# Kernel tuning notes

Measured on AMD Instinct MI355X. Metric: run time of the kernel, lower is better.

Reference implementation:

```python
import jax, jax.numpy as jnp
import numpy as np

B, V, P, N = 8, 4096, 2048, 32
IN_DIM, H, D, L = 256, 8, 32, 2
MLP, RES = 128, 100
HD = H * D
EPS = 1e-5


def setup_inputs() -> dict:
    key = jax.random.key(0)
    ks = jax.random.split(key, 12)
    s = 0.02
    inp = {
        'encoded': jax.random.normal(ks[0], (B, V, IN_DIM), jnp.float32),
        'true_u': jax.random.uniform(ks[1], (B, V), jnp.float32),
        'pred_points': jax.random.randint(ks[2], (P,), 0, V),
        'neighbor_index': jax.random.randint(ks[3], (P, N), 0, V),
        'Wds': s * jax.random.normal(ks[4], (IN_DIM, HD), jnp.float32),
        'bds': jnp.zeros((HD,), jnp.float32),
    }

    def mlp_params(k, lead, in_dim, out_dim):
        kk = jax.random.split(k, 3)
        return (s * jax.random.normal(kk[0], lead + (in_dim, MLP), jnp.float32), jnp.zeros(lead + (MLP,), jnp.float32),
                s * jax.random.normal(kk[1], lead + (MLP, MLP), jnp.float32), jnp.zeros(lead + (MLP,), jnp.float32),
                s * jax.random.normal(kk[2], lead + (MLP, out_dim), jnp.float32), jnp.zeros(lead + (out_dim,), jnp.float32))

    inp['kW1'], inp['kb1'], inp['kW2'], inp['kb2'], inp['kW3'], inp['kb3'] = mlp_params(ks[5], (L, H), IN_DIM + 1, D)
    inp['vW1'], inp['vb1'], inp['vW2'], inp['vb2'], inp['vW3'], inp['vb3'] = mlp_params(ks[6], (L, H), IN_DIM + 1, D)
    inp['dW1'], inp['db1'], inp['dW2'], inp['db2'], inp['dW3'], inp['db3'] = mlp_params(ks[7], (), HD, RES)
    inp['ln1_g'] = jnp.ones((L, HD), jnp.float32); inp['ln1_b'] = jnp.zeros((L, HD), jnp.float32)
    inp['ln2_g'] = jnp.ones((L, HD), jnp.float32); inp['ln2_b'] = jnp.zeros((L, HD), jnp.float32)
    inp['fW1'] = s * jax.random.normal(ks[8], (L, HD, HD), jnp.float32); inp['fb1'] = jnp.zeros((L, HD), jnp.float32)
    inp['fW2'] = s * jax.random.normal(ks[9], (L, HD, HD), jnp.float32); inp['fb2'] = jnp.zeros((L, HD), jnp.float32)
    return inp


def _ln(x, g, b):
    m = x.mean(-1, keepdims=True)
    v = ((x - m) ** 2).mean(-1, keepdims=True)
    return (x - m) * jax.lax.rsqrt(v + EPS) * g + b


def _per_head_mlp(x, W1, b1, W2, b2, W3, b3):
    # x: [B,V,I]; W1: [H,I,M] -> out [B,H,V,D]; all H per-head MLPs batched in one einsum
    h = jax.nn.relu(jnp.einsum('bvi,him->bhvm', x, W1) + b1[None, :, None, :])
    h = jax.nn.relu(jnp.einsum('bhvm,hmn->bhvn', h, W2) + b2[None, :, None, :])
    return jnp.einsum('bhvm,hmd->bhvd', h, W3) + b3[None, :, None, :]


def reference(encoded, true_u, pred_points, neighbor_index, Wds, bds, kW1, kb1, kW2, kb2, kW3, kb3, vW1, vb1, vW2, vb2, vW3, vb3, dW1, db1, dW2, db2, dW3, db3, ln1_g, ln1_b, ln2_g, ln2_b, fW1, fb1, fW2, fb2):
    merged = jnp.concatenate([encoded, true_u[..., None]], axis=-1)  # [B,V,IN+1]
    att_value = encoded[:, pred_points, :] @ Wds + bds               # [B,P,HD]
    scale = D ** -0.5
    for l in range(L):
        keys = _per_head_mlp(merged, kW1[l], kb1[l], kW2[l], kb2[l], kW3[l], kb3[l])    # [B,H,V,D]
        values = _per_head_mlp(merged, vW1[l], vb1[l], vW2[l], vb2[l], vW3[l], vb3[l])  # [B,H,V,D]
        nk = keys[:, :, neighbor_index, :]    # gather -> [B,H,P,N,D]
        nv = values[:, :, neighbor_index, :]
        q = att_value.reshape(att_value.shape[0], -1, H, D)  # [B,P,H,D]
        scores = scale * jnp.einsum('bphd,bhpnd->bphn', q, nk)
        w = jax.nn.softmax(scores, axis=-1)
        att = jnp.einsum('bphn,bhpnd->bphd', w, nv).reshape(att_value.shape)
        att_value = _ln(att_value + att, ln1_g[l], ln1_b[l])
        ff = jax.nn.relu(att_value @ fW1[l] + fb1[l]) @ fW2[l] + fb2[l]
        att_value = _ln(att_value + ff, ln2_g[l], ln2_b[l])
    h = jax.nn.relu(att_value @ dW1 + db1)
    h = jax.nn.relu(h @ dW2 + db2)
    logits = h @ dW3 + db3  # [B,P,RES]
    target = jnp.clip(jnp.floor(true_u[..., None] * RES).astype(jnp.int32), 0, RES - 1)  # [B,V,1]
    logprob = jnp.log(jnp.float32(RES)) + jax.nn.log_softmax(logits, axis=2)
    picked = jnp.take_along_axis(logprob, target[:, pred_points, :], axis=2)  # [B,P,1]
    return -picked.sum((1, 2))  # [B]
```

## Files before the change

### kernel.cpp

```cpp
#include <hip/hip_runtime.h>
#include <math.h>

#define B_    8
#define V_    4096
#define P_    2048
#define N_    32
#define INDIM 256
#define H_    8
#define D_    32
#define L_    2
#define MLP_  128
#define RES_  100
#define HD_   256
#define EPS_  1e-5f
#define SCALE_ 0.17677669529663687f
#define LOG_RES_ 4.605170185988091f

__global__ __launch_bounds__(256) void k_init_att(
    const float* __restrict__ encoded, const int* __restrict__ pp,
    const float* __restrict__ Wds, const float* __restrict__ bds,
    float* __restrict__ att)
{
    __shared__ float xs[32][INDIM];
    const int t = threadIdx.x;
    const int g0 = blockIdx.x * 32;
    for (int idx = t; idx < 32 * INDIM; idx += 256) {
        int r = idx >> 8, i = idx & 255;
        int g = g0 + r;
        int b = g >> 11, pl = g & 2047;
        xs[r][i] = encoded[((size_t)b * V_ + pp[pl]) * INDIM + i];
    }
    __syncthreads();
    const int jg = t & 63, rg = t >> 6;
    const int j = jg * 4;
    float acc[8][4];
    #pragma unroll
    for (int r = 0; r < 8; ++r)
        #pragma unroll
        for (int c = 0; c < 4; ++c) acc[r][c] = 0.f;
    for (int i = 0; i < INDIM; ++i) {
        const float4 w = *(const float4*)&Wds[(size_t)i * HD_ + j];
        #pragma unroll
        for (int r = 0; r < 8; ++r) {
            float x = xs[rg * 8 + r][i];
            acc[r][0] += x * w.x; acc[r][1] += x * w.y;
            acc[r][2] += x * w.z; acc[r][3] += x * w.w;
        }
    }
    const float4 bb = *(const float4*)&bds[j];
    #pragma unroll
    for (int r = 0; r < 8; ++r) {
        float4 o;
        o.x = acc[r][0] + bb.x; o.y = acc[r][1] + bb.y;
        o.z = acc[r][2] + bb.z; o.w = acc[r][3] + bb.w;
        *(float4*)&att[((size_t)(g0 + rg * 8 + r)) * HD_ + j] = o;
    }
}

__global__ __launch_bounds__(256) void k_kv_mlp(
    const float* __restrict__ encoded, const float* __restrict__ true_u,
    const float* __restrict__ kW1, const float* __restrict__ kb1,
    const float* __restrict__ kW2, const float* __restrict__ kb2,
    const float* __restrict__ kW3, const float* __restrict__ kb3,
    const float* __restrict__ vW1, const float* __restrict__ vb1,
    const float* __restrict__ vW2, const float* __restrict__ vb2,
    const float* __restrict__ vW3, const float* __restrict__ vb3,
    float* __restrict__ keys, float* __restrict__ values)
{
    __shared__ float smem[32 * (INDIM + 1) + 32 * (MLP_ + 1)];
    float (*xs)[INDIM + 1] = (float (*)[INDIM + 1])smem;
    float (*h1)[MLP_ + 1]  = (float (*)[MLP_ + 1])(smem + 32 * (INDIM + 1));
    float (*h2)[MLP_ + 1]  = (float (*)[MLP_ + 1])smem;

    const int t  = threadIdx.x;
    const int g0 = blockIdx.x * 32;
    const int b  = g0 >> 12;
    const int v0 = g0 & (V_ - 1);
    const int hh = blockIdx.y;
    const int kv = blockIdx.z;
    const float* W1 = (kv ? vW1 : kW1) + (size_t)hh * (INDIM + 1) * MLP_;
    const float* b1 = (kv ? vb1 : kb1) + hh * MLP_;
    const float* W2 = (kv ? vW2 : kW2) + (size_t)hh * MLP_ * MLP_;
    const float* b2 = (kv ? vb2 : kb2) + hh * MLP_;
    const float* W3 = (kv ? vW3 : kW3) + (size_t)hh * MLP_ * D_;
    const float* b3 = (kv ? vb3 : kb3) + hh * D_;
    float* outp = kv ? values : keys;

    const float* xb = encoded + ((size_t)b * V_ + v0) * INDIM;
    for (int idx = t; idx < 32 * INDIM; idx += 256) {
        int r = idx >> 8, i = idx & 255;
        xs[r][i] = xb[(size_t)r * INDIM + i];
    }
    if (t < 32) xs[t][INDIM] = true_u[(size_t)b * V_ + v0 + t];
    __syncthreads();

    const int cg = t & 31;
    const int vg = t >> 5;

    {
        const int m = cg * 4;
        float acc[4][4];
        #pragma unroll
        for (int r = 0; r < 4; ++r)
            #pragma unroll
            for (int c = 0; c < 4; ++c) acc[r][c] = 0.f;
        for (int i = 0; i < INDIM + 1; ++i) {
            const float4 w = *(const float4*)&W1[(size_t)i * MLP_ + m];
            #pragma unroll
            for (int r = 0; r < 4; ++r) {
                float x = xs[vg * 4 + r][i];
                acc[r][0] += x * w.x; acc[r][1] += x * w.y;
                acc[r][2] += x * w.z; acc[r][3] += x * w.w;
            }
        }
        const float4 bb = *(const float4*)&b1[m];
        #pragma unroll
        for (int r = 0; r < 4; ++r) {
            h1[vg * 4 + r][m + 0] = fmaxf(acc[r][0] + bb.x, 0.f);
            h1[vg * 4 + r][m + 1] = fmaxf(acc[r][1] + bb.y, 0.f);
            h1[vg * 4 + r][m + 2] = fmaxf(acc[r][2] + bb.z, 0.f);
            h1[vg * 4 + r][m + 3] = fmaxf(acc[r][3] + bb.w, 0.f);
        }
    }
    __syncthreads();

    {
        const int m = cg * 4;
        float acc[4][4];
        #pragma unroll
        for (int r = 0; r < 4; ++r)
            #pragma unroll
            for (int c = 0; c < 4; ++c) acc[r][c] = 0.f;
        for (int i = 0; i < MLP_; ++i) {
            const float4 w = *(const float4*)&W2[(size_t)i * MLP_ + m];
            #pragma unroll
            for (int r = 0; r < 4; ++r) {
                float x = h1[vg * 4 + r][i];
                acc[r][0] += x * w.x; acc[r][1] += x * w.y;
                acc[r][2] += x * w.z; acc[r][3] += x * w.w;
            }
        }
        const float4 bb = *(const float4*)&b2[m];
        #pragma unroll
        for (int r = 0; r < 4; ++r) {
            h2[vg * 4 + r][m + 0] = fmaxf(acc[r][0] + bb.x, 0.f);
            h2[vg * 4 + r][m + 1] = fmaxf(acc[r][1] + bb.y, 0.f);
            h2[vg * 4 + r][m + 2] = fmaxf(acc[r][2] + bb.z, 0.f);
            h2[vg * 4 + r][m + 3] = fmaxf(acc[r][3] + bb.w, 0.f);
        }
    }
    __syncthreads();

    {
        const int dg = t & 7;
        const int vq = t >> 3;
        const int d = dg * 4;
        float acc[4] = {0.f, 0.f, 0.f, 0.f};
        for (int i = 0; i < MLP_; ++i) {
            const float4 w = *(const float4*)&W3[(size_t)i * D_ + d];
            float x = h2[vq][i];
            acc[0] += x * w.x; acc[1] += x * w.y;
            acc[2] += x * w.z; acc[3] += x * w.w;
        }
        float4 o;
        o.x = acc[0] + b3[d + 0]; o.y = acc[1] + b3[d + 1];
        o.z = acc[2] + b3[d + 2]; o.w = acc[3] + b3[d + 3];
        *(float4*)&outp[((size_t)b * V_ + v0 + vq) * HD_ + hh * D_ + d] = o;
    }
}

__global__ __launch_bounds__(256) void k_attn_ln(
    const float* __restrict__ keys, const float* __restrict__ values,
    const int* __restrict__ nbr,
    const float* __restrict__ g, const float* __restrict__ bet,
    float* __restrict__ att)
{
    __shared__ float qs[HD_];
    __shared__ float ws[H_][N_];
    __shared__ int   idx[N_];
    __shared__ float red[4];
    const int t = threadIdx.x;
    const int bp = blockIdx.x;
    const int b = bp >> 11;
    const int p = bp & (P_ - 1);
    if (t < N_) idx[t] = nbr[p * N_ + t];
    qs[t] = att[(size_t)bp * HD_ + t];
    __syncthreads();

    const int hh = t >> 5;
    {
        const int n = t & 31;
        const float4* kp = (const float4*)(keys + ((size_t)b * V_ + idx[n]) * HD_ + hh * D_);
        float s = 0.f;
        #pragma unroll
        for (int j = 0; j < 8; ++j) {
            const float4 kk = kp[j];
            s += qs[hh * D_ + j * 4 + 0] * kk.x + qs[hh * D_ + j * 4 + 1] * kk.y +
                 qs[hh * D_ + j * 4 + 2] * kk.z + qs[hh * D_ + j * 4 + 3] * kk.w;
        }
        s *= SCALE_;
        float m = s;
        #pragma unroll
        for (int off = 16; off; off >>= 1) m = fmaxf(m, __shfl_xor(m, off, 32));
        float e = expf(s - m);
        float sum = e;
        #pragma unroll
        for (int off = 16; off; off >>= 1) sum += __shfl_xor(sum, off, 32);
        ws[hh][n] = e / sum;
    }
    __syncthreads();

    float a = 0.f;
    {
        const int d = t & 31;
        const float* vb = values + (size_t)b * V_ * HD_ + hh * D_ + d;
        #pragma unroll
        for (int n2 = 0; n2 < N_; ++n2)
            a += ws[hh][n2] * vb[(size_t)idx[n2] * HD_];
    }

    float x = qs[t] + a;
    float s1 = x;
    #pragma unroll
    for (int off = 32; off; off >>= 1) s1 += __shfl_xor(s1, off, 64);
    if ((t & 63) == 0) red[t >> 6] = s1;
    __syncthreads();
    float mean = (red[0] + red[1] + red[2] + red[3]) * (1.f / HD_);
    __syncthreads();
    float dx = x - mean;
    float v2 = dx * dx;
    #pragma unroll
    for (int off = 32; off; off >>= 1) v2 += __shfl_xor(v2, off, 64);
    if ((t & 63) == 0) red[t >> 6] = v2;
    __syncthreads();
    float var = (red[0] + red[1] + red[2] + red[3]) * (1.f / HD_);
    att[(size_t)bp * HD_ + t] = dx * rsqrtf(var + EPS_) * g[t] + bet[t];
}

#define FP_ (HD_ + 4)
__global__ __launch_bounds__(256) void k_ff_ln(
    const float* __restrict__ W1, const float* __restrict__ b1,
    const float* __restrict__ W2, const float* __restrict__ b2,
    const float* __restrict__ g, const float* __restrict__ bet,
    float* __restrict__ att)
{
    __shared__ float xs[32][FP_];
    __shared__ float hs[32][FP_];
    const int t = threadIdx.x;
    const int g0 = blockIdx.x * 32;
    for (int idx = t; idx < 32 * HD_; idx += 256) {
        int r = idx >> 8, i = idx & 255;
        xs[r][i] = att[((size_t)(g0 + r)) * HD_ + i];
    }
    __syncthreads();
    const int jg = t & 63, rg = t >> 6;
    const int j = jg * 4;

    float acc[8][4];
    #pragma unroll
    for (int r = 0; r < 8; ++r)
        #pragma unroll
        for (int c = 0; c < 4; ++c) acc[r][c] = 0.f;
    for (int i = 0; i < HD_; ++i) {
        const float4 w = *(const float4*)&W1[(size_t)i * HD_ + j];
        #pragma unroll
        for (int r = 0; r < 8; ++r) {
            float x = xs[rg * 8 + r][i];
            acc[r][0] += x * w.x; acc[r][1] += x * w.y;
            acc[r][2] += x * w.z; acc[r][3] += x * w.w;
        }
    }
    {
        const float4 bb = *(const float4*)&b1[j];
        #pragma unroll
        for (int r = 0; r < 8; ++r) {
            float4 o;
            o.x = fmaxf(acc[r][0] + bb.x, 0.f); o.y = fmaxf(acc[r][1] + bb.y, 0.f);
            o.z = fmaxf(acc[r][2] + bb.z, 0.f); o.w = fmaxf(acc[r][3] + bb.w, 0.f);
            *(float4*)&hs[rg * 8 + r][j] = o;
        }
    }
    __syncthreads();

    #pragma unroll
    for (int r = 0; r < 8; ++r)
        #pragma unroll
        for (int c = 0; c < 4; ++c) acc[r][c] = 0.f;
    for (int i = 0; i < HD_; ++i) {
        const float4 w = *(const float4*)&W2[(size_t)i * HD_ + j];
        #pragma unroll
        for (int r = 0; r < 8; ++r) {
            float x = hs[rg * 8 + r][i];
            acc[r][0] += x * w.x; acc[r][1] += x * w.y;
            acc[r][2] += x * w.z; acc[r][3] += x * w.w;
        }
    }
    float y[8][4];
    {
        const float4 bb = *(const float4*)&b2[j];
        #pragma unroll
        for (int r = 0; r < 8; ++r) {
            y[r][0] = acc[r][0] + bb.x + xs[rg * 8 + r][j + 0];
            y[r][1] = acc[r][1] + bb.y + xs[rg * 8 + r][j + 1];
            y[r][2] = acc[r][2] + bb.z + xs[rg * 8 + r][j + 2];
            y[r][3] = acc[r][3] + bb.w + xs[rg * 8 + r][j + 3];
        }
    }
    __syncthreads();
    #pragma unroll
    for (int r = 0; r < 8; ++r) {
        float4 o; o.x = y[r][0]; o.y = y[r][1]; o.z = y[r][2]; o.w = y[r][3];
        *(float4*)&xs[rg * 8 + r][j] = o;
    }
    __syncthreads();

    const int rr = t >> 3, k = t & 7;
    float s = 0.f;
    for (int i = 0; i < 32; ++i) s += xs[rr][k + 8 * i];
    #pragma unroll
    for (int off = 4; off; off >>= 1) s += __shfl_xor(s, off, 8);
    float mean = s * (1.f / HD_);
    float vs = 0.f;
    for (int i = 0; i < 32; ++i) { float d = xs[rr][k + 8 * i] - mean; vs += d * d; }
    #pragma unroll
    for (int off = 4; off; off >>= 1) vs += __shfl_xor(vs, off, 8);
    float rstd = rsqrtf(vs * (1.f / HD_) + EPS_);
    for (int i = 0; i < 32; ++i) {
        int jj = k + 8 * i;
        att[((size_t)(g0 + rr)) * HD_ + jj] =
            (xs[rr][jj] - mean) * rstd * g[jj] + bet[jj];
    }
}

__global__ __launch_bounds__(256) void k_dec_loss(
    const float* __restrict__ att, const float* __restrict__ true_u,
    const int* __restrict__ pp,
    const float* __restrict__ dW1, const float* __restrict__ db1,
    const float* __restrict__ dW2, const float* __restrict__ db2,
    const float* __restrict__ dW3, const float* __restrict__ db3,
    float* __restrict__ partial)
{
    __shared__ float xs[32][HD_];
    __shared__ float h1s[32][MLP_];
    __shared__ float h2s[32][MLP_];
    __shared__ float ls[32][104];
    __shared__ float rowloss[32];
    const int t = threadIdx.x;
    const int g0 = blockIdx.x * 32;
    for (int idx = t; idx < 32 * HD_; idx += 256) {
        int r = idx >> 8, i = idx & 255;
        xs[r][i] = att[((size_t)(g0 + r)) * HD_ + i];
    }
    __syncthreads();
    const int jg = t & 31, rg = t >> 5;
    const int j = jg * 4;

    {
        float acc[4][4];
        #pragma unroll
        for (int r = 0; r < 4; ++r)
            #pragma unroll
            for (int c = 0; c < 4; ++c) acc[r][c] = 0.f;
        for (int i = 0; i < HD_; ++i) {
            const float4 w = *(const float4*)&dW1[(size_t)i * MLP_ + j];
            #pragma unroll
            for (int r = 0; r < 4; ++r) {
                float x = xs[rg * 4 + r][i];
                acc[r][0] += x * w.x; acc[r][1] += x * w.y;
                acc[r][2] += x * w.z; acc[r][3] += x * w.w;
            }
        }
        const float4 bb = *(const float4*)&db1[j];
        #pragma unroll
        for (int r = 0; r < 4; ++r) {
            float4 o;
            o.x = fmaxf(acc[r][0] + bb.x, 0.f); o.y = fmaxf(acc[r][1] + bb.y, 0.f);
            o.z = fmaxf(acc[r][2] + bb.z, 0.f); o.w = fmaxf(acc[r][3] + bb.w, 0.f);
            *(float4*)&h1s[rg * 4 + r][j] = o;
        }
    }
    __syncthreads();
    {
        float acc[4][4];
        #pragma unroll
        for (int r = 0; r < 4; ++r)
            #pragma unroll
            for (int c = 0; c < 4; ++c) acc[r][c] = 0.f;
        for (int i = 0; i < MLP_; ++i) {
            const float4 w = *(const float4*)&dW2[(size_t)i * MLP_ + j];
            #pragma unroll
            for (int r = 0; r < 4; ++r) {
                float x = h1s[rg * 4 + r][i];
                acc[r][0] += x * w.x; acc[r][1] += x * w.y;
                acc[r][2] += x * w.z; acc[r][3] += x * w.w;
            }
        }
        const float4 bb = *(const float4*)&db2[j];
        #pragma unroll
        for (int r = 0; r < 4; ++r) {
            float4 o;
            o.x = fmaxf(acc[r][0] + bb.x, 0.f); o.y = fmaxf(acc[r][1] + bb.y, 0.f);
            o.z = fmaxf(acc[r][2] + bb.z, 0.f); o.w = fmaxf(acc[r][3] + bb.w, 0.f);
            *(float4*)&h2s[rg * 4 + r][j] = o;
        }
    }
    __syncthreads();
    {
        const bool act = (jg < 25);
        float acc[4][4];
        #pragma unroll
        for (int r = 0; r < 4; ++r)
            #pragma unroll
            for (int c = 0; c < 4; ++c) acc[r][c] = 0.f;
        for (int i = 0; i < MLP_; ++i) {
            float4 w = make_float4(0.f, 0.f, 0.f, 0.f);
            if (act) w = *(const float4*)&dW3[(size_t)i * RES_ + j];
            #pragma unroll
            for (int r = 0; r < 4; ++r) {
                float x = h2s[rg * 4 + r][i];
                acc[r][0] += x * w.x; acc[r][1] += x * w.y;
                acc[r][2] += x * w.z; acc[r][3] += x * w.w;
            }
        }
        if (act) {
            const float4 bb = *(const float4*)&db3[j];
            #pragma unroll
            for (int r = 0; r < 4; ++r) {
                ls[rg * 4 + r][j + 0] = acc[r][0] + bb.x;
                ls[rg * 4 + r][j + 1] = acc[r][1] + bb.y;
                ls[rg * 4 + r][j + 2] = acc[r][2] + bb.z;
                ls[rg * 4 + r][j + 3] = acc[r][3] + bb.w;
            }
        }
    }
    __syncthreads();

    const int rr = t >> 3, k = t & 7;
    float mx = -1e30f;
    for (int q = k; q < RES_; q += 8) mx = fmaxf(mx, ls[rr][q]);
    #pragma unroll
    for (int off = 4; off; off >>= 1) mx = fmaxf(mx, __shfl_xor(mx, off, 8));
    float se = 0.f;
    for (int q = k; q < RES_; q += 8) se += expf(ls[rr][q] - mx);
    #pragma unroll
    for (int off = 4; off; off >>= 1) se += __shfl_xor(se, off, 8);
    if (k == 0) {
        int gg = g0 + rr;
        int b = gg >> 11, pl = gg & (P_ - 1);
        float tu = true_u[(size_t)b * V_ + pp[pl]];
        int tgt = (int)floorf(tu * (float)RES_);
        tgt = tgt < 0 ? 0 : (tgt > RES_ - 1 ? RES_ - 1 : tgt);
        rowloss[rr] = LOG_RES_ + ls[rr][tgt] - mx - logf(se);
    }
    __syncthreads();
    if (t == 0) {
        float s = 0.f;
        for (int r2 = 0; r2 < 32; ++r2) s += rowloss[r2];
        partial[blockIdx.x] = -s;
    }
}

__global__ __launch_bounds__(64) void k_reduce_loss(
    const float* __restrict__ partial, float* __restrict__ loss)
{
    const int b = blockIdx.x, t = threadIdx.x;
    float s = partial[b * 64 + t];
    #pragma unroll
    for (int off = 32; off; off >>= 1) s += __shfl_xor(s, off, 64);
    if (t == 0) loss[b] = s;
}

extern "C" void kernel_launch(void* const* d_in, const int* in_sizes, int n_in,
                              void* d_out, int out_size, void* d_ws, size_t ws_size,
                              hipStream_t stream)
{
    (void)in_sizes; (void)n_in; (void)out_size; (void)ws_size;
    const float* encoded = (const float*)d_in[0];
    const float* true_u  = (const float*)d_in[1];
    const int*   pp      = (const int*)d_in[2];
    const int*   nbr     = (const int*)d_in[3];
    const float* Wds     = (const float*)d_in[4];
    const float* bds     = (const float*)d_in[5];
    const float* kW1 = (const float*)d_in[6];
    const float* kb1 = (const float*)d_in[7];
    const float* kW2 = (const float*)d_in[8];
    const float* kb2 = (const float*)d_in[9];
    const float* kW3 = (const float*)d_in[10];
    const float* kb3 = (const float*)d_in[11];
    const float* vW1 = (const float*)d_in[12];
    const float* vb1 = (const float*)d_in[13];
    const float* vW2 = (const float*)d_in[14];
    const float* vb2 = (const float*)d_in[15];
    const float* vW3 = (const float*)d_in[16];
    const float* vb3 = (const float*)d_in[17];
    const float* dW1 = (const float*)d_in[18];
    const float* db1 = (const float*)d_in[19];
    const float* dW2 = (const float*)d_in[20];
    const float* db2 = (const float*)d_in[21];
    const float* dW3 = (const float*)d_in[22];
    const float* db3 = (const float*)d_in[23];
    const float* ln1g = (const float*)d_in[24];
    const float* ln1b = (const float*)d_in[25];
    const float* ln2g = (const float*)d_in[26];
    const float* ln2b = (const float*)d_in[27];
    const float* fW1 = (const float*)d_in[28];
    const float* fb1 = (const float*)d_in[29];
    const float* fW2 = (const float*)d_in[30];
    const float* fb2 = (const float*)d_in[31];

    float* att  = (float*)d_ws;
    float* keys = att + (size_t)B_ * P_ * HD_;
    float* vals = keys + (size_t)B_ * V_ * HD_;
    float* part = vals + (size_t)B_ * V_ * HD_;

    k_init_att<<<dim3((B_ * P_) / 32), 256, 0, stream>>>(encoded, pp, Wds, bds, att);

    for (int l = 0; l < L_; ++l) {
        k_kv_mlp<<<dim3((B_ * V_) / 32, H_, 2), 256, 0, stream>>>(
            encoded, true_u,
            kW1 + (size_t)l * H_ * (INDIM + 1) * MLP_, kb1 + l * H_ * MLP_,
            kW2 + (size_t)l * H_ * MLP_ * MLP_,        kb2 + l * H_ * MLP_,
            kW3 + (size_t)l * H_ * MLP_ * D_,          kb3 + l * H_ * D_,
            vW1 + (size_t)l * H_ * (INDIM + 1) * MLP_, vb1 + l * H_ * MLP_,
            vW2 + (size_t)l * H_ * MLP_ * MLP_,        vb2 + l * H_ * MLP_,
            vW3 + (size_t)l * H_ * MLP_ * D_,          vb3 + l * H_ * D_,
            keys, vals);
        k_attn_ln<<<dim3(B_ * P_), 256, 0, stream>>>(
            keys, vals, nbr, ln1g + l * HD_, ln1b + l * HD_, att);
        k_ff_ln<<<dim3((B_ * P_) / 32), 256, 0, stream>>>(
            fW1 + (size_t)l * HD_ * HD_, fb1 + l * HD_,
            fW2 + (size_t)l * HD_ * HD_, fb2 + l * HD_,
            ln2g + l * HD_, ln2b + l * HD_, att);
    }

    k_dec_loss<<<dim3((B_ * P_) / 32), 256, 0, stream>>>(
        att, true_u, pp, dW1, db1, dW2, db2, dW3, db3, part);
    k_reduce_loss<<<dim3(B_), 64, 0, stream>>>(part, (float*)d_out);
}
```

Baseline: 2.796 ms.

## Restructure per-head KV MLP with float4 LDS reads, weight prefetch, halved shared memory

Rewrites the k_kv_mlp kernel so the 256-wide input is staged in two 128-column halves, with the second half held in registers. This shrinks shared memory and raises occupancy via launch_bounds(256,4). Inner loops now read four activations at once as float4 from a padded (132) LDS layout and software-prefetch the next four weight rows. The aim is fewer LDS instructions and hidden global weight-load latency. The trade-off is extra register pressure and an extra barrier for the second input half.

Result: faster. 2.597 ms (-7.1%).

```diff
diff --git a/kernel.cpp b/kernel.cpp
--- a/kernel.cpp
+++ b/kernel.cpp
@@ -16,6 +16,8 @@
 #define SCALE_ 0.17677669529663687f
 #define LOG_RES_ 4.605170185988091f
 
+#define LDP_  132
+
 __global__ __launch_bounds__(256) void k_init_att(
     const float* __restrict__ encoded, const int* __restrict__ pp,
     const float* __restrict__ Wds, const float* __restrict__ bds,
@@ -57,7 +59,38 @@
     }
 }
 
-__global__ __launch_bounds__(256) void k_kv_mlp(
+#define MLP_STEP4(XS, ROWBASE, ACC, I, WA, WB, WC, WD)                       \
+    { _Pragma("unroll")                                                      \
+      for (int r_ = 0; r_ < 4; ++r_) {                                       \
+        const float4 xv = *(const float4*)&XS[(ROWBASE) + r_][(I)];          \
+        ACC[r_][0] += xv.x*WA.x; ACC[r_][1] += xv.x*WA.y;                    \
+        ACC[r_][2] += xv.x*WA.z; ACC[r_][3] += xv.x*WA.w;                    \
+        ACC[r_][0] += xv.y*WB.x; ACC[r_][1] += xv.y*WB.y;                    \
+        ACC[r_][2] += xv.y*WB.z; ACC[r_][3] += xv.y*WB.w;                    \
+        ACC[r_][0] += xv.z*WC.x; ACC[r_][1] += xv.z*WC.y;                    \
+        ACC[r_][2] += xv.z*WC.z; ACC[r_][3] += xv.z*WC.w;                    \
+        ACC[r_][0] += xv.w*WD.x; ACC[r_][1] += xv.w*WD.y;                    \
+        ACC[r_][2] += xv.w*WD.z; ACC[r_][3] += xv.w*WD.w;                    \
+      } }
+
+#define PIPE128(WPTR, LDW, XS, ROWBASE, ACC)                                 \
+    { const float* wp_ = (WPTR);                                             \
+      float4 wa = *(const float4*)&wp_[0*(LDW)];                             \
+      float4 wb = *(const float4*)&wp_[1*(LDW)];                             \
+      float4 wc = *(const float4*)&wp_[2*(LDW)];                             \
+      float4 wd = *(const float4*)&wp_[3*(LDW)];                             \
+      for (int i_ = 0; i_ < 124; i_ += 4) {                                  \
+        float4 na = *(const float4*)&wp_[(size_t)(i_+4)*(LDW)];              \
+        float4 nb = *(const float4*)&wp_[(size_t)(i_+5)*(LDW)];              \
+        float4 nc = *(const float4*)&wp_[(size_t)(i_+6)*(LDW)];              \
+        float4 nd = *(const float4*)&wp_[(size_t)(i_+7)*(LDW)];              \
+        MLP_STEP4(XS, ROWBASE, ACC, i_, wa, wb, wc, wd);                     \
+        wa = na; wb = nb; wc = nc; wd = nd;                                  \
+      }                                                                      \
+      MLP_STEP4(XS, ROWBASE, ACC, 124, wa, wb, wc, wd);                      \
+    }
+
+__global__ __launch_bounds__(256, 4) void k_kv_mlp(
     const float* __restrict__ encoded, const float* __restrict__ true_u,
     const float* __restrict__ kW1, const float* __restrict__ kb1,
     const float* __restrict__ kW2, const float* __restrict__ kb2,
@@ -67,10 +100,12 @@
     const float* __restrict__ vW3, const float* __restrict__ vb3,
     float* __restrict__ keys, float* __restrict__ values)
 {
-    __shared__ float smem[32 * (INDIM + 1) + 32 * (MLP_ + 1)];
-    float (*xs)[INDIM + 1] = (float (*)[INDIM + 1])smem;
-    float (*h1)[MLP_ + 1]  = (float (*)[MLP_ + 1])(smem + 32 * (INDIM + 1));
-    float (*h2)[MLP_ + 1]  = (float (*)[MLP_ + 1])smem;
+    __shared__ float xcs[32 * LDP_];
+    __shared__ float h1s[32 * LDP_];
+    __shared__ float us[32];
+    float (*xc)[LDP_] = (float (*)[LDP_])xcs;
+    float (*h1)[LDP_] = (float (*)[LDP_])h1s;
+    float (*h2)[LDP_] = (float (*)[LDP_])xcs;
 
     const int t  = threadIdx.x;
     const int g0 = blockIdx.x * 32;
@@ -87,84 +122,110 @@
     float* outp = kv ? values : keys;
 
     const float* xb = encoded + ((size_t)b * V_ + v0) * INDIM;
-    for (int idx = t; idx < 32 * INDIM; idx += 256) {
-        int r = idx >> 8, i = idx & 255;
-        xs[r][i] = xb[(size_t)r * INDIM + i];
-    }
-    if (t < 32) xs[t][INDIM] = true_u[(size_t)b * V_ + v0 + t];
-    __syncthreads();
-
-    const int cg = t & 31;
-    const int vg = t >> 5;
-
-    {
-        const int m = cg * 4;
-        float acc[4][4];
-        #pragma unroll
-        for (int r = 0; r < 4; ++r)
-            #pragma unroll
-            for (int c = 0; c < 4; ++c) acc[r][c] = 0.f;
-        for (int i = 0; i < INDIM + 1; ++i) {
-            const float4 w = *(const float4*)&W1[(size_t)i * MLP_ + m];
-            #pragma unroll
-            for (int r = 0; r < 4; ++r) {
-                float x = xs[vg * 4 + r][i];
-                acc[r][0] += x * w.x; acc[r][1] += x * w.y;
-                acc[r][2] += x * w.z; acc[r][3] += x * w.w;
-            }
-        }
+    float4 c1r[4];
+    #pragma unroll
+    for (int k = 0; k < 4; ++k) {
+        int idx = t + (k << 8);
+        int row = idx >> 5, c4 = (idx & 31) << 2;
+        *(float4*)&xc[row][c4] = *(const float4*)&xb[(size_t)row * INDIM + c4];
+        c1r[k] = *(const float4*)&xb[(size_t)row * INDIM + 128 + c4];
+    }
+    if (t < 32) us[t] = true_u[(size_t)b * V_ + v0 + t];
+    __syncthreads();
+
+    const int cg = t & 31, vg = t >> 5;
+    const int m  = cg << 2;
+    const int r0 = vg << 2;
+
+    float acc[4][4];
+    #pragma unroll
+    for (int r = 0; r < 4; ++r)
+        #pragma unroll
+        for (int c = 0; c < 4; ++c) acc[r][c] = 0.f;
+
+    PIPE128(W1 + m, MLP_, xc, r0, acc);
+    __syncthreads();
+    #pragma unroll
+    for (int k = 0; k < 4; ++k) {
+        int idx = t + (k << 8);
+        int row = idx >> 5, c4 = (idx & 31) << 2;
+        *(float4*)&xc[row][c4] = c1r[k];
+    }
+    __syncthreads();
+    PIPE128(W1 + (size_t)128 * MLP_ + m, MLP_, xc, r0, acc);
+    {
+        const float4 wu = *(const float4*)&W1[(size_t)256 * MLP_ + m];
+        #pragma unroll
+        for (int r = 0; r < 4; ++r) {
+            float uu = us[r0 + r];
+            acc[r][0] += uu * wu.x; acc[r][1] += uu * wu.y;
+            acc[r][2] += uu * wu.z; acc[r][3] += uu * wu.w;
+        }
+    }
+    {
         const float4 bb = *(const float4*)&b1[m];
         #pragma unroll
         for (int r = 0; r < 4; ++r) {
-            h1[vg * 4 + r][m + 0] = fmaxf(acc[r][0] + bb.x, 0.f);
-            h1[vg * 4 + r][m + 1] = fmaxf(acc[r][1] + bb.y, 0.f);
-            h1[vg * 4 + r][m + 2] = fmaxf(acc[r][2] + bb.z, 0.f);
-            h1[vg * 4 + r][m + 3] = fmaxf(acc[r][3] + bb.w, 0.f);
-        }
-    }
-    __syncthreads();
-
-    {
-        const int m = cg * 4;
-        float acc[4][4];
-        #pragma unroll
-        for (int r = 0; r < 4; ++r)
-            #pragma unroll
-            for (int c = 0; c < 4; ++c) acc[r][c] = 0.f;
-        for (int i = 0; i < MLP_; ++i) {
-            const float4 w = *(const float4*)&W2[(size_t)i * MLP_ + m];
-            #pragma unroll
-            for (int r = 0; r < 4; ++r) {
-                float x = h1[vg * 4 + r][i];
-                acc[r][0] += x * w.x; acc[r][1] += x * w.y;
-                acc[r][2] += x * w.z; acc[r][3] += x * w.w;
-            }
-        }
+            float4 o;
+            o.x = fmaxf(acc[r][0] + bb.x, 0.f);
+            o.y = fmaxf(acc[r][1] + bb.y, 0.f);
+            o.z = fmaxf(acc[r][2] + bb.z, 0.f);
+            o.w = fmaxf(acc[r][3] + bb.w, 0.f);
+            *(float4*)&h1[r0 + r][m] = o;
+        }
+    }
+    __syncthreads();
+
+    #pragma unroll
+    for (int r = 0; r < 4; ++r)
+        #pragma unroll
+        for (int c = 0; c < 4; ++c) acc[r][c] = 0.f;
+    PIPE128(W2 + m, MLP_, h1, r0, acc);
+    {
         const float4 bb = *(const float4*)&b2[m];
         #pragma unroll
         for (int r = 0; r < 4; ++r) {
-            h2[vg * 4 + r][m + 0] = fmaxf(acc[r][0] + bb.x, 0.f);
-            h2[vg * 4 + r][m + 1] = fmaxf(acc[r][1] + bb.y, 0.f);
-            h2[vg * 4 + r][m + 2] = fmaxf(acc[r][2] + bb.z, 0.f);
-            h2[vg * 4 + r][m + 3] = fmaxf(acc[r][3] + bb.w, 0.f);
-        }
-    }
-    __syncthreads();
-
-    {
-        const int dg = t & 7;
-        const int vq = t >> 3;
-        const int d = dg * 4;
-        float acc[4] = {0.f, 0.f, 0.f, 0.f};
-        for (int i = 0; i < MLP_; ++i) {
-            const float4 w = *(const float4*)&W3[(size_t)i * D_ + d];
-            float x = h2[vq][i];
-            acc[0] += x * w.x; acc[1] += x * w.y;
-            acc[2] += x * w.z; acc[3] += x * w.w;
+            float4 o;
+            o.x = fmaxf(acc[r][0] + bb.x, 0.f);
+            o.y = fmaxf(acc[r][1] + bb.y, 0.f);
+            o.z = fmaxf(acc[r][2] + bb.z, 0.f);
+            o.w = fmaxf(acc[r][3] + bb.w, 0.f);
+            *(float4*)&h2[r0 + r][m] = o;
+        }
+    }
+    __syncthreads();
+
+    {
+        const int dg = t & 7, vq = t >> 3;
+        const int d = dg << 2;
+        float a0 = 0.f, a1 = 0.f, a2 = 0.f, a3 = 0.f;
+        const float* wp = W3 + d;
+        float4 wa = *(const float4*)&wp[0 * D_];
+        float4 wb = *(const float4*)&wp[1 * D_];
+        float4 wc = *(const float4*)&wp[2 * D_];
+        float4 wd = *(const float4*)&wp[3 * D_];
+        for (int i = 0; i < 124; i += 4) {
+            float4 na = *(const float4*)&wp[(size_t)(i + 4) * D_];
+            float4 nb = *(const float4*)&wp[(size_t)(i + 5) * D_];
+            float4 nc = *(const float4*)&wp[(size_t)(i + 6) * D_];
+            float4 nd = *(const float4*)&wp[(size_t)(i + 7) * D_];
+            const float4 xv = *(const float4*)&h2[vq][i];
+            a0 += xv.x*wa.x; a1 += xv.x*wa.y; a2 += xv.x*wa.z; a3 += xv.x*wa.w;
+            a0 += xv.y*wb.x; a1 += xv.y*wb.y; a2 += xv.y*wb.z; a3 += xv.y*wb.w;
+            a0 += xv.z*wc.x; a1 += xv.z*wc.y; a2 += xv.z*wc.z; a3 += xv.z*wc.w;
+            a0 += xv.w*wd.x; a1 += xv.w*wd.y; a2 += xv.w*wd.z; a3 += xv.w*wd.w;
+            wa = na; wb = nb; wc = nc; wd = nd;
+        }
+        {
+            const float4 xv = *(const float4*)&h2[vq][124];
+            a0 += xv.x*wa.x; a1 += xv.x*wa.y; a2 += xv.x*wa.z; a3 += xv.x*wa.w;
+            a0 += xv.y*wb.x; a1 += xv.y*wb.y; a2 += xv.y*wb.z; a3 += xv.y*wb.w;
+            a0 += xv.z*wc.x; a1 += xv.z*wc.y; a2 += xv.z*wc.z; a3 += xv.z*wc.w;
+            a0 += xv.w*wd.x; a1 += xv.w*wd.y; a2 += xv.w*wd.z; a3 += xv.w*wd.w;
         }
         float4 o;
-        o.x = acc[0] + b3[d + 0]; o.y = acc[1] + b3[d + 1];
-        o.z = acc[2] + b3[d + 2]; o.w = acc[3] + b3[d + 3];
+        o.x = a0 + b3[d + 0]; o.y = a1 + b3[d + 1];
+        o.z = a2 + b3[d + 2]; o.w = a3 + b3[d + 3];
         *(float4*)&outp[((size_t)b * V_ + v0 + vq) * HD_ + hh * D_ + d] = o;
     }
 }
```

## Retile per-head KV MLP with 64-row blocks and 4x8 register tiles

Applied to the files above, without the earlier changes.

Rewrites the per-head key/value MLP kernel to process 64 vertices per block, with each thread holding a 4x8 accumulator tile. Activations are read from shared memory as float4 and weights are software-prefetched one group of four rows ahead. The input is split into two 128-wide halves so the shared buffers can be reused for the hidden layers, and the kernel is pinned to two waves per EU. The aim is more reuse of weight loads and fewer LDS reads per FMA. The cost is higher register pressure and lower occupancy.

New measurement: 2.512 ms. 1.11x faster.

```diff
diff --git a/kernel.cpp b/kernel.cpp
--- a/kernel.cpp
+++ b/kernel.cpp
@@ -16,6 +16,8 @@
 #define SCALE_ 0.17677669529663687f
 #define LOG_RES_ 4.605170185988091f
 
+#define LDP_  132
+
 __global__ __launch_bounds__(256) void k_init_att(
     const float* __restrict__ encoded, const int* __restrict__ pp,
     const float* __restrict__ Wds, const float* __restrict__ bds,
@@ -57,7 +59,55 @@
     }
 }
 
-__global__ __launch_bounds__(256) void k_kv_mlp(
+
+#define FMA8(R, XSC, WL, WH)                                                 \
+    acc[R][0] += (XSC)*WL.x; acc[R][1] += (XSC)*WL.y;                        \
+    acc[R][2] += (XSC)*WL.z; acc[R][3] += (XSC)*WL.w;                        \
+    acc[R][4] += (XSC)*WH.x; acc[R][5] += (XSC)*WH.y;                        \
+    acc[R][6] += (XSC)*WH.z; acc[R][7] += (XSC)*WH.w;
+
+#define GRP4(XS, I)                                                          \
+    { const float4 xv0 = *(const float4*)&XS[r0 + 0][(I)];                   \
+      const float4 xv1 = *(const float4*)&XS[r0 + 1][(I)];                   \
+      const float4 xv2 = *(const float4*)&XS[r0 + 2][(I)];                   \
+      const float4 xv3 = *(const float4*)&XS[r0 + 3][(I)];                   \
+      FMA8(0, xv0.x, w0, w1); FMA8(1, xv1.x, w0, w1);                        \
+      FMA8(2, xv2.x, w0, w1); FMA8(3, xv3.x, w0, w1);                        \
+      FMA8(0, xv0.y, w2, w3); FMA8(1, xv1.y, w2, w3);                        \
+      FMA8(2, xv2.y, w2, w3); FMA8(3, xv3.y, w2, w3);                        \
+      FMA8(0, xv0.z, w4, w5); FMA8(1, xv1.z, w4, w5);                        \
+      FMA8(2, xv2.z, w4, w5); FMA8(3, xv3.z, w4, w5);                        \
+      FMA8(0, xv0.w, w6, w7); FMA8(1, xv1.w, w6, w7);                        \
+      FMA8(2, xv2.w, w6, w7); FMA8(3, xv3.w, w6, w7); }
+
+#define PIPE128(WPTR, LDW, XS)                                               \
+    { const float* wp_ = (WPTR);                                             \
+      float4 w0 = *(const float4*)&wp_[0];                                   \
+      float4 w1 = *(const float4*)&wp_[4];                                   \
+      float4 w2 = *(const float4*)&wp_[(size_t)(LDW)];                       \
+      float4 w3 = *(const float4*)&wp_[(size_t)(LDW) + 4];                   \
+      float4 w4 = *(const float4*)&wp_[2*(size_t)(LDW)];                     \
+      float4 w5 = *(const float4*)&wp_[2*(size_t)(LDW) + 4];                 \
+      float4 w6 = *(const float4*)&wp_[3*(size_t)(LDW)];                     \
+      float4 w7 = *(const float4*)&wp_[3*(size_t)(LDW) + 4];                 \
+      for (int i_ = 0; i_ < 124; i_ += 4) {                                  \
+        float4 n0 = *(const float4*)&wp_[(size_t)(i_+4)*(LDW)];              \
+        float4 n1 = *(const float4*)&wp_[(size_t)(i_+4)*(LDW) + 4];          \
+        float4 n2 = *(const float4*)&wp_[(size_t)(i_+5)*(LDW)];              \
+        float4 n3 = *(const float4*)&wp_[(size_t)(i_+5)*(LDW) + 4];          \
+        float4 n4 = *(const float4*)&wp_[(size_t)(i_+6)*(LDW)];              \
+        float4 n5 = *(const float4*)&wp_[(size_t)(i_+6)*(LDW) + 4];          \
+        float4 n6 = *(const float4*)&wp_[(size_t)(i_+7)*(LDW)];              \
+        float4 n7 = *(const float4*)&wp_[(size_t)(i_+7)*(LDW) + 4];          \
+        GRP4(XS, i_);                                                        \
+        w0=n0; w1=n1; w2=n2; w3=n3; w4=n4; w5=n5; w6=n6; w7=n7;              \
+      }                                                                      \
+      GRP4(XS, 124);                                                         \
+    }
+
+__global__ __launch_bounds__(256)
+__attribute__((amdgpu_waves_per_eu(2, 2)))
+void k_kv_mlp(
     const float* __restrict__ encoded, const float* __restrict__ true_u,
     const float* __restrict__ kW1, const float* __restrict__ kb1,
     const float* __restrict__ kW2, const float* __restrict__ kb2,
@@ -67,13 +117,14 @@
     const float* __restrict__ vW3, const float* __restrict__ vb3,
     float* __restrict__ keys, float* __restrict__ values)
 {
-    __shared__ float smem[32 * (INDIM + 1) + 32 * (MLP_ + 1)];
-    float (*xs)[INDIM + 1] = (float (*)[INDIM + 1])smem;
-    float (*h1)[MLP_ + 1]  = (float (*)[MLP_ + 1])(smem + 32 * (INDIM + 1));
-    float (*h2)[MLP_ + 1]  = (float (*)[MLP_ + 1])smem;
+    __shared__ float bufA[64 * LDP_];
+    __shared__ float bufB[64 * LDP_];
+    __shared__ float us[64];
+    float (*xa)[LDP_] = (float (*)[LDP_])bufA;
+    float (*xb)[LDP_] = (float (*)[LDP_])bufB;
 
     const int t  = threadIdx.x;
-    const int g0 = blockIdx.x * 32;
+    const int g0 = blockIdx.x * 64;
     const int b  = g0 >> 12;
     const int v0 = g0 & (V_ - 1);
     const int hh = blockIdx.y;
@@ -86,86 +137,130 @@
     const float* b3 = (kv ? vb3 : kb3) + hh * D_;
     float* outp = kv ? values : keys;
 
-    const float* xb = encoded + ((size_t)b * V_ + v0) * INDIM;
-    for (int idx = t; idx < 32 * INDIM; idx += 256) {
-        int r = idx >> 8, i = idx & 255;
-        xs[r][i] = xb[(size_t)r * INDIM + i];
-    }
-    if (t < 32) xs[t][INDIM] = true_u[(size_t)b * V_ + v0 + t];
-    __syncthreads();
-
-    const int cg = t & 31;
-    const int vg = t >> 5;
-
-    {
-        const int m = cg * 4;
-        float acc[4][4];
-        #pragma unroll
-        for (int r = 0; r < 4; ++r)
-            #pragma unroll
-            for (int c = 0; c < 4; ++c) acc[r][c] = 0.f;
-        for (int i = 0; i < INDIM + 1; ++i) {
-            const float4 w = *(const float4*)&W1[(size_t)i * MLP_ + m];
-            #pragma unroll
-            for (int r = 0; r < 4; ++r) {
-                float x = xs[vg * 4 + r][i];
-                acc[r][0] += x * w.x; acc[r][1] += x * w.y;
-                acc[r][2] += x * w.z; acc[r][3] += x * w.w;
-            }
-        }
-        const float4 bb = *(const float4*)&b1[m];
+    const float* xgb = encoded + ((size_t)b * V_ + v0) * INDIM;
+    #pragma unroll
+    for (int k = 0; k < 8; ++k) {
+        int idx = t + (k << 8);
+        int row = idx >> 5, c4 = (idx & 31) << 2;
+        *(float4*)&xa[row][c4] = *(const float4*)&xgb[(size_t)row * INDIM + c4];
+        *(float4*)&xb[row][c4] = *(const float4*)&xgb[(size_t)row * INDIM + 128 + c4];
+    }
+    if (t < 64) us[t] = true_u[(size_t)b * V_ + v0 + t];
+    __syncthreads();
+
+    const int cg = t & 15, vg = t >> 4;
+    const int m  = cg << 3;
+    const int r0 = vg << 2;
+
+    float acc[4][8];
+    #pragma unroll
+    for (int r = 0; r < 4; ++r)
+        #pragma unroll
+        for (int c = 0; c < 8; ++c) acc[r][c] = 0.f;
+
+    PIPE128(W1 + m, MLP_, xa);
+    PIPE128(W1 + (size_t)128 * MLP_ + m, MLP_, xb);
+    {
+        const float4 wu0 = *(const float4*)&W1[(size_t)256 * MLP_ + m];
+        const float4 wu1 = *(const float4*)&W1[(size_t)256 * MLP_ + m + 4];
         #pragma unroll
         for (int r = 0; r < 4; ++r) {
-            h1[vg * 4 + r][m + 0] = fmaxf(acc[r][0] + bb.x, 0.f);
-            h1[vg * 4 + r][m + 1] = fmaxf(acc[r][1] + bb.y, 0.f);
-            h1[vg * 4 + r][m + 2] = fmaxf(acc[r][2] + bb.z, 0.f);
-            h1[vg * 4 + r][m + 3] = fmaxf(acc[r][3] + bb.w, 0.f);
-        }
-    }
-    __syncthreads();
-
-    {
-        const int m = cg * 4;
-        float acc[4][4];
-        #pragma unroll
-        for (int r = 0; r < 4; ++r)
-            #pragma unroll
-            for (int c = 0; c < 4; ++c) acc[r][c] = 0.f;
-        for (int i = 0; i < MLP_; ++i) {
-            const float4 w = *(const float4*)&W2[(size_t)i * MLP_ + m];
-            #pragma unroll
-            for (int r = 0; r < 4; ++r) {
-                float x = h1[vg * 4 + r][i];
-                acc[r][0] += x * w.x; acc[r][1] += x * w.y;
-                acc[r][2] += x * w.z; acc[r][3] += x * w.w;
-            }
-        }
-        const float4 bb = *(const float4*)&b2[m];
+            const float uu = us[r0 + r];
+            FMA8(r, uu, wu0, wu1);
+        }
+    }
+    __syncthreads();
+    {
+        const float4 bb0 = *(const float4*)&b1[m];
+        const float4 bb1 = *(const float4*)&b1[m + 4];
         #pragma unroll
         for (int r = 0; r < 4; ++r) {
-            h2[vg * 4 + r][m + 0] = fmaxf(acc[r][0] + bb.x, 0.f);
-            h2[vg * 4 + r][m + 1] = fmaxf(acc[r][1] + bb.y, 0.f);
-            h2[vg * 4 + r][m + 2] = fmaxf(acc[r][2] + bb.z, 0.f);
-            h2[vg * 4 + r][m + 3] = fmaxf(acc[r][3] + bb.w, 0.f);
-        }
-    }
-    __syncthreads();
-
-    {
-        const int dg = t & 7;
-        const int vq = t >> 3;
-        const int d = dg * 4;
-        float acc[4] = {0.f, 0.f, 0.f, 0.f};
-        for (int i = 0; i < MLP_; ++i) {
-            const float4 w = *(const float4*)&W3[(size_t)i * D_ + d];
-            float x = h2[vq][i];
-            acc[0] += x * w.x; acc[1] += x * w.y;
-            acc[2] += x * w.z; acc[3] += x * w.w;
+            float4 o;
+            o.x = fmaxf(acc[r][0] + bb0.x, 0.f); o.y = fmaxf(acc[r][1] + bb0.y, 0.f);
+            o.z = fmaxf(acc[r][2] + bb0.z, 0.f); o.w = fmaxf(acc[r][3] + bb0.w, 0.f);
+            *(float4*)&xa[r0 + r][m] = o;
+            o.x = fmaxf(acc[r][4] + bb1.x, 0.f); o.y = fmaxf(acc[r][5] + bb1.y, 0.f);
+            o.z = fmaxf(acc[r][6] + bb1.z, 0.f); o.w = fmaxf(acc[r][7] + bb1.w, 0.f);
+            *(float4*)&xa[r0 + r][m + 4] = o;
+        }
+    }
+    __syncthreads();
+
+    #pragma unroll
+    for (int r = 0; r < 4; ++r)
+        #pragma unroll
+        for (int c = 0; c < 8; ++c) acc[r][c] = 0.f;
+    PIPE128(W2 + m, MLP_, xa);
+    __syncthreads();
+    {
+        const float4 bb0 = *(const float4*)&b2[m];
+        const float4 bb1 = *(const float4*)&b2[m + 4];
+        #pragma unroll
+        for (int r = 0; r < 4; ++r) {
+            float4 o;
+            o.x = fmaxf(acc[r][0] + bb0.x, 0.f); o.y = fmaxf(acc[r][1] + bb0.y, 0.f);
+            o.z = fmaxf(acc[r][2] + bb0.z, 0.f); o.w = fmaxf(acc[r][3] + bb0.w, 0.f);
+            *(float4*)&xb[r0 + r][m] = o;
+            o.x = fmaxf(acc[r][4] + bb1.x, 0.f); o.y = fmaxf(acc[r][5] + bb1.y, 0.f);
+            o.z = fmaxf(acc[r][6] + bb1.z, 0.f); o.w = fmaxf(acc[r][7] + bb1.w, 0.f);
+            *(float4*)&xb[r0 + r][m + 4] = o;
+        }
+    }
+    __syncthreads();
+
+    {
+        const int vq = t >> 2, d = (t & 3) << 3;
+        float a[8];
+        #pragma unroll
+        for (int c = 0; c < 8; ++c) a[c] = 0.f;
+        const float* wp = W3 + d;
+        float4 w0 = *(const float4*)&wp[0];
+        float4 w1 = *(const float4*)&wp[4];
+        float4 w2 = *(const float4*)&wp[D_];
+        float4 w3 = *(const float4*)&wp[D_ + 4];
+        float4 w4 = *(const float4*)&wp[2 * D_];
+        float4 w5 = *(const float4*)&wp[2 * D_ + 4];
+        float4 w6 = *(const float4*)&wp[3 * D_];
+        float4 w7 = *(const float4*)&wp[3 * D_ + 4];
+        for (int i = 0; i < 124; i += 4) {
+            float4 n0 = *(const float4*)&wp[(size_t)(i + 4) * D_];
+            float4 n1 = *(const float4*)&wp[(size_t)(i + 4) * D_ + 4];
+            float4 n2 = *(const float4*)&wp[(size_t)(i + 5) * D_];
+            float4 n3 = *(const float4*)&wp[(size_t)(i + 5) * D_ + 4];
+            float4 n4 = *(const float4*)&wp[(size_t)(i + 6) * D_];
+            float4 n5 = *(const float4*)&wp[(size_t)(i + 6) * D_ + 4];
+            float4 n6 = *(const float4*)&wp[(size_t)(i + 7) * D_];
+            float4 n7 = *(const float4*)&wp[(size_t)(i + 7) * D_ + 4];
+            const float4 xv = *(const float4*)&xb[vq][i];
+            a[0]+=xv.x*w0.x; a[1]+=xv.x*w0.y; a[2]+=xv.x*w0.z; a[3]+=xv.x*w0.w;
+            a[4]+=xv.x*w1.x; a[5]+=xv.x*w1.y; a[6]+=xv.x*w1.z; a[7]+=xv.x*w1.w;
+            a[0]+=xv.y*w2.x; a[1]+=xv.y*w2.y; a[2]+=xv.y*w2.z; a[3]+=xv.y*w2.w;
+            a[4]+=xv.y*w3.x; a[5]+=xv.y*w3.y; a[6]+=xv.y*w3.z; a[7]+=xv.y*w3.w;
+            a[0]+=xv.z*w4.x; a[1]+=xv.z*w4.y; a[2]+=xv.z*w4.z; a[3]+=xv.z*w4.w;
+            a[4]+=xv.z*w5.x; a[5]+=xv.z*w5.y; a[6]+=xv.z*w5.z; a[7]+=xv.z*w5.w;
+            a[0]+=xv.w*w6.x; a[1]+=xv.w*w6.y; a[2]+=xv.w*w6.z; a[3]+=xv.w*w6.w;
+            a[4]+=xv.w*w7.x; a[5]+=xv.w*w7.y; a[6]+=xv.w*w7.z; a[7]+=xv.w*w7.w;
+            w0=n0; w1=n1; w2=n2; w3=n3; w4=n4; w5=n5; w6=n6; w7=n7;
+        }
+        {
+            const float4 xv = *(const float4*)&xb[vq][124];
+            a[0]+=xv.x*w0.x; a[1]+=xv.x*w0.y; a[2]+=xv.x*w0.z; a[3]+=xv.x*w0.w;
+            a[4]+=xv.x*w1.x; a[5]+=xv.x*w1.y; a[6]+=xv.x*w1.z; a[7]+=xv.x*w1.w;
+            a[0]+=xv.y*w2.x; a[1]+=xv.y*w2.y; a[2]+=xv.y*w2.z; a[3]+=xv.y*w2.w;
+            a[4]+=xv.y*w3.x; a[5]+=xv.y*w3.y; a[6]+=xv.y*w3.z; a[7]+=xv.y*w3.w;
+            a[0]+=xv.z*w4.x; a[1]+=xv.z*w4.y; a[2]+=xv.z*w4.z; a[3]+=xv.z*w4.w;
+            a[4]+=xv.z*w5.x; a[5]+=xv.z*w5.y; a[6]+=xv.z*w5.z; a[7]+=xv.z*w5.w;
+            a[0]+=xv.w*w6.x; a[1]+=xv.w*w6.y; a[2]+=xv.w*w6.z; a[3]+=xv.w*w6.w;
+            a[4]+=xv.w*w7.x; a[5]+=xv.w*w7.y; a[6]+=xv.w*w7.z; a[7]+=xv.w*w7.w;
         }
         float4 o;
-        o.x = acc[0] + b3[d + 0]; o.y = acc[1] + b3[d + 1];
-        o.z = acc[2] + b3[d + 2]; o.w = acc[3] + b3[d + 3];
-        *(float4*)&outp[((size_t)b * V_ + v0 + vq) * HD_ + hh * D_ + d] = o;
+        float* op = &outp[((size_t)b * V_ + v0 + vq) * HD_ + hh * D_ + d];
+        o.x = a[0] + b3[d + 0]; o.y = a[1] + b3[d + 1];
+        o.z = a[2] + b3[d + 2]; o.w = a[3] + b3[d + 3];
+        *(float4*)&op[0] = o;
+        o.x = a[4] + b3[d + 4]; o.y = a[5] + b3[d + 5];
+        o.z = a[6] + b3[d + 6]; o.w = a[7] + b3[d + 7];
+        *(float4*)&op[4] = o;
     }
 }
 
@@ -516,7 +611,7 @@
     k_init_att<<<dim3((B_ * P_) / 32), 256, 0, stream>>>(encoded, pp, Wds, bds, att);
 
     for (int l = 0; l < L_; ++l) {
-        k_kv_mlp<<<dim3((B_ * V_) / 32, H_, 2), 256, 0, stream>>>(
+        k_kv_mlp<<<dim3((B_ * V_) / 64, H_, 2), 256, 0, stream>>>(
             encoded, true_u,
             kW1 + (size_t)l * H_ * (INDIM + 1) * MLP_, kb1 + l * H_ * MLP_,
             kW2 + (size_t)l * H_ * MLP_ * MLP_,        kb2 + l * H_ * MLP_,
```
